# Kernel optimization log

Measured on AMD Instinct MI355X. Metric: run time of the kernel, lower is better.

Reference implementation:

```python
import jax, jax.numpy as jnp
import numpy as np

B, N = 4, 1024                 # images, proposals per image
C_IN, POOL, HID = 256, 7, 1024
NUM_CLASSES = 21               # 20 fg + background (include_bg=False => +1)
FEAT_DIM = C_IN * POOL * POOL  # 12544
IMAGE_H = IMAGE_W = 800.0
STDS = np.array([0.1, 0.1, 0.2, 0.2], np.float32)
SCORE_THRESH = 0.1
NMS_THRESH = 0.5


def setup_inputs():
    key = jax.random.key(0)
    ks = jax.random.split(key, 11)
    props_feature = jax.random.normal(ks[0], (B * N, FEAT_DIM), jnp.float32)
    # well-formed xyxy proposals inside the image
    xy = jax.random.uniform(ks[1], (B, N, 2), minval=0.0, maxval=IMAGE_W - 64.0)
    wh = jax.random.uniform(ks[2], (B, N, 2), minval=8.0, maxval=256.0)
    proposals = jnp.concatenate([xy, jnp.minimum(xy + wh, IMAGE_W)], axis=-1)
    s = 0.02
    return {
        'props_feature': props_feature,
        'proposals': proposals,
        'fc6_w': jax.random.normal(ks[3], (FEAT_DIM, HID), jnp.float32) * s,
        'fc6_b': jnp.zeros((HID,), jnp.float32),
        'fc7_w': jax.random.normal(ks[4], (HID, HID), jnp.float32) * s,
        'fc7_b': jnp.zeros((HID,), jnp.float32),
        'cls_w': jax.random.normal(ks[5], (HID, NUM_CLASSES), jnp.float32) * s,
        'cls_b': jnp.zeros((NUM_CLASSES,), jnp.float32),
        'box_w': jax.random.normal(ks[6], (HID, NUM_CLASSES * 4), jnp.float32) * s,
        'box_b': jnp.zeros((NUM_CLASSES * 4,), jnp.float32),
    }


def _decode(deltas, props):
    # NormalizedProposalDecoder: deltas [...,4] (normalized), props xyxy [...,4]
    d = deltas * jnp.asarray(STDS)  # means are 0
    w = props[..., 2] - props[..., 0]
    h = props[..., 3] - props[..., 1]
    cx = props[..., 0] + 0.5 * w
    cy = props[..., 1] + 0.5 * h
    pcx = d[..., 0] * w + cx
    pcy = d[..., 1] * h + cy
    pw = jnp.exp(d[..., 2]) * w
    ph = jnp.exp(d[..., 3]) * h
    return jnp.stack([pcx - 0.5 * pw, pcy - 0.5 * ph,
                      pcx + 0.5 * pw, pcy + 0.5 * ph], axis=-1)


def _pairwise_iou(a, b):
    lt = jnp.maximum(a[:, None, :2], b[None, :, :2])
    rb = jnp.minimum(a[:, None, 2:], b[None, :, 2:])
    wh = jnp.maximum(rb - lt, 0.0)
    inter = wh[..., 0] * wh[..., 1]
    area_a = (a[:, 2] - a[:, 0]) * (a[:, 3] - a[:, 1])
    area_b = (b[:, 2] - b[:, 0]) * (b[:, 3] - b[:, 1])
    return inter / jnp.maximum(area_a[:, None] + area_b[None, :] - inter, 1e-9)


def _nms_keep(boxes, scores, labels, valid):
    # torchvision batched_nms: per-class via coordinate offset trick
    sc = jnp.where(valid, scores, -1.0)
    order = jnp.argsort(-sc)
    off = labels[order].astype(boxes.dtype)[:, None] * (IMAGE_W + 1.0)
    b = boxes[order] + off
    iou = _pairwise_iou(b, b)  # [N, N]
    idx = jnp.arange(N)

    def body(i, keep):
        sup = (iou[i] > NMS_THRESH) & keep[i] & (idx > i)
        return keep & ~sup

    keep_sorted = jax.lax.fori_loop(0, N, body, valid[order])
    return jnp.zeros(N, bool).at[order].set(keep_sorted)


def reference(props_feature, proposals, fc6_w, fc6_b, fc7_w, fc7_b,
              cls_w, cls_b, box_w, box_b):
    # TwoMLPHead
    x = jax.nn.relu(props_feature @ fc6_w + fc6_b)
    x = jax.nn.relu(x @ fc7_w + fc7_b)
    # FastRCNNPredictor
    scores = jax.nn.softmax(x @ cls_w + cls_b, axis=-1).reshape(B, N, NUM_CLASSES)
    deltas = (x @ box_w + box_b).reshape(B, N, NUM_CLASSES, 4)
    boxes = _decode(deltas, proposals[:, :, None, :])  # [B,N,C,4]
    # drop background column, keep per-box max-score class (scores == max mask)
    sc_fg = scores[..., 1:]
    bx_fg = boxes[:, :, 1:, :]
    best = jnp.argmax(sc_fg, axis=-1)                                  # [B,N]
    sc = jnp.take_along_axis(sc_fg, best[..., None], axis=-1)[..., 0]
    bx = jnp.take_along_axis(bx_fg, best[..., None, None], axis=-2)[..., 0, :]
    labels = best + 1
    # BBoxClipToImageSize
    hi = jnp.asarray([IMAGE_W, IMAGE_H, IMAGE_W, IMAGE_H], bx.dtype)
    bx = jnp.clip(bx, jnp.zeros(4, bx.dtype), hi)
    # BBoxSizeFilter(min=0) + score threshold
    valid = ((bx[..., 2] - bx[..., 0] > 0.0) & (bx[..., 3] - bx[..., 1] > 0.0)
             & (sc > SCORE_THRESH))
    keep = jax.vmap(_nms_keep)(bx, sc, labels, valid)                  # [B,N]
    res = jnp.concatenate([bx, (labels - 1).astype(bx.dtype)[..., None],
                           sc[..., None]], axis=-1)                    # [B,N,6]
    res = jnp.where(keep[..., None], res, 0.0)  # padded in place of ragged lists
    rpn_props = jnp.pad(proposals, ((0, 0), (0, 0), (0, 2)))
    rcnn_props = jnp.pad(bx, ((0, 0), (0, 0), (0, 2)))
    return res, keep, rpn_props, rcnn_props
```

## Files before the change

### kernel.cpp

```cpp
#include <hip/hip_runtime.h>
#include <hip/hip_bf16.h>

#define BATCH 4
#define NPROP 1024
#define HID 1024
#define NUM_CLASSES 21
#define FEAT_DIM 12544
#define NPB (BATCH * NPROP)
#define IMG 800.0f
#define SCORE_THRESH 0.1f
#define NMS_THRESH 0.5f
#define NCOL 112

typedef unsigned short u16;
typedef unsigned int u32;
typedef unsigned long long u64;
typedef short s16x8 __attribute__((ext_vector_type(8)));
typedef float f32x4 __attribute__((ext_vector_type(4)));

__device__ __forceinline__ void split2(float x0, float x1, u32& hp, u32& lp) {
    __hip_bfloat162 h2 = __float22bfloat162_rn(make_float2(x0, x1));
    u32 h = *(u32*)&h2;
    float f0 = __uint_as_float(h << 16);
    float f1 = __uint_as_float(h & 0xffff0000u);
    __hip_bfloat162 l2 = __float22bfloat162_rn(make_float2(x0 - f0, x1 - f1));
    hp = h;
    lp = *(u32*)&l2;
}

__device__ __forceinline__ size_t tile_off(int blk, int NTt, int t, int row, int g) {
    int r = row & 127;
    int c = r >> 4;
    int lanei = ((r & 15) << 2) | (g ^ ((r >> 1) & 3));
    return ((((size_t)blk * NTt + t) * 8 + c) << 9) + lanei * 8;
}

__global__ __launch_bounds__(256) void transpose_split(
    const float* __restrict__ W, u16* __restrict__ WhT, u16* __restrict__ WlT,
    int K, int N)
{
    __shared__ float tile[32][33];
    const int tid = threadIdx.x;
    const int n0 = blockIdx.x * 32;
    const int k0 = blockIdx.y * 32;
    {
        int i = tid >> 3, j4 = (tid & 7) * 4;
        float4 v = *(const float4*)(W + (size_t)(k0 + i) * N + n0 + j4);
        tile[i][j4] = v.x; tile[i][j4 + 1] = v.y; tile[i][j4 + 2] = v.z; tile[i][j4 + 3] = v.w;
    }
    __syncthreads();
    {
        int i = tid >> 3, j4 = (tid & 7) * 4;
        u32 hp0, lp0, hp1, lp1;
        split2(tile[j4 + 0][i], tile[j4 + 1][i], hp0, lp0);
        split2(tile[j4 + 2][i], tile[j4 + 3][i], hp1, lp1);
        size_t o = (size_t)(n0 + i) * K + k0 + j4;
        *(uint2*)&WhT[o] = make_uint2(hp0, hp1);
        *(uint2*)&WlT[o] = make_uint2(lp0, lp1);
    }
}

__global__ __launch_bounds__(256) void transpose_split_tiled(
    const float* __restrict__ W, u16* __restrict__ Th, u16* __restrict__ Tl,
    int K, int N)
{
    __shared__ float tile[32][33];
    const int tid = threadIdx.x;
    const int n0 = blockIdx.x * 32;
    const int k0 = blockIdx.y * 32;
    {
        int i = tid >> 3, j4 = (tid & 7) * 4;
        float4 v = *(const float4*)(W + (size_t)(k0 + i) * N + n0 + j4);
        tile[i][j4] = v.x; tile[i][j4 + 1] = v.y; tile[i][j4 + 2] = v.z; tile[i][j4 + 3] = v.w;
    }
    __syncthreads();
    if (tid < 128) {
        const int nl = tid & 31, g = tid >> 5;
        const int n = n0 + nl;
        u32 hp[4], lp[4];
#pragma unroll
        for (int e2 = 0; e2 < 4; ++e2)
            split2(tile[g * 8 + e2 * 2][nl], tile[g * 8 + e2 * 2 + 1][nl], hp[e2], lp[e2]);
        size_t dsto = tile_off(n >> 7, K >> 5, k0 >> 5, n, g);
        *(uint4*)&Th[dsto] = make_uint4(hp[0], hp[1], hp[2], hp[3]);
        *(uint4*)&Tl[dsto] = make_uint4(lp[0], lp[1], lp[2], lp[3]);
    }
}

__global__ __launch_bounds__(256) void split_a_tiled(
    const float* __restrict__ A, u16* __restrict__ Ah, u16* __restrict__ Al,
    int K, long n8)
{
    const int NTt = K >> 5;
    for (long i = blockIdx.x * 256L + threadIdx.x; i < n8; i += (long)gridDim.x * 256L) {
        size_t o = (size_t)i * 8;
        int row = (int)(o / (size_t)K);
        int rem = (int)(o - (size_t)row * K);
        int t = rem >> 5;
        int g = (rem >> 3) & 3;
        float4 v0 = *(const float4*)(A + o);
        float4 v1 = *(const float4*)(A + o + 4);
        u32 hp[4], lp[4];
        split2(v0.x, v0.y, hp[0], lp[0]);
        split2(v0.z, v0.w, hp[1], lp[1]);
        split2(v1.x, v1.y, hp[2], lp[2]);
        split2(v1.z, v1.w, hp[3], lp[3]);
        size_t dsto = tile_off(row >> 7, NTt, t, row, g);
        *(uint4*)&Ah[dsto] = make_uint4(hp[0], hp[1], hp[2], hp[3]);
        *(uint4*)&Al[dsto] = make_uint4(lp[0], lp[1], lp[2], lp[3]);
    }
}

__global__ void build_wcat(const float* __restrict__ cls_w, const float* __restrict__ box_w,
                           float* __restrict__ Wcat)
{
    int i = blockIdx.x * 256 + threadIdx.x;
    if (i >= HID * NCOL) return;
    int k = i / NCOL, c = i % NCOL;
    float v = 0.0f;
    if (c < 21) v = cls_w[k * 21 + c];
    else if (c < 105) v = box_w[k * 84 + (c - 21)];
    Wcat[i] = v;
}

__global__ __launch_bounds__(256) void gemm_2ph_tiled(
    const u16* __restrict__ Ah, const u16* __restrict__ Al,
    const u16* __restrict__ Wh, const u16* __restrict__ Wl,
    const float* __restrict__ bias, float* __restrict__ Cout,
    int M, int Nn, int NTt, int tN)
{
    __shared__ u16 sm[2 * 16384];

    const int tid = threadIdx.x;
    const int lane = tid & 63;
    const int wv = tid >> 6;
    const int wr = wv >> 1, wc = wv & 1;

    const int flat = blockIdx.x + (blockIdx.y << 3) + (blockIdx.z << 8);
    const int xcd = flat & 7;
    const int j = flat >> 3;
    const int bxi = j & 7;
    const int yy = (j >> 3) & 3;
    const int bz = j >> 5;
    const int mb = xcd * 4 + yy;
    const int nb = bxi;
    const int bm = mb * 128, bn = nb * 128;
    const int t0 = bz * tN;

    const size_t abase = (size_t)mb * NTt * 4096;
    const size_t wbase = (size_t)nb * NTt * 4096;

    const int fr = lane & 15, fq = lane >> 4;
    int ia[4], ib[4];
#pragma unroll
    for (int m = 0; m < 4; ++m) {
        int ra = wr * 64 + m * 16 + fr;
        ia[m] = ra * 32 + ((fq ^ ((ra >> 1) & 3)) << 3);
        int rb = wc * 64 + m * 16 + fr;
        ib[m] = rb * 32 + ((fq ^ ((rb >> 1) & 3)) << 3);
    }

    f32x4 acc[4][4];
#pragma unroll
    for (int m = 0; m < 4; ++m)
#pragma unroll
        for (int n = 0; n < 4; ++n)
            acc[m][n] = (f32x4){0.f, 0.f, 0.f, 0.f};

    auto stage = [&](u16* dst, int t) {
#pragma unroll
        for (int i = 0; i < 2; ++i) {
            const int c = wv * 2 + i;
            const size_t so = (((size_t)t * 8 + c) << 9) + lane * 8;
            __builtin_amdgcn_global_load_lds(
                (const __attribute__((address_space(1))) u32*)(Ah + abase + so),
                (__attribute__((address_space(3))) u32*)(dst + c * 512), 16, 0, 0);
            __builtin_amdgcn_global_load_lds(
                (const __attribute__((address_space(1))) u32*)(Al + abase + so),
                (__attribute__((address_space(3))) u32*)(dst + 4096 + c * 512), 16, 0, 0);
            __builtin_amdgcn_global_load_lds(
                (const __attribute__((address_space(1))) u32*)(Wh + wbase + so),
                (__attribute__((address_space(3))) u32*)(dst + 8192 + c * 512), 16, 0, 0);
            __builtin_amdgcn_global_load_lds(
                (const __attribute__((address_space(1))) u32*)(Wl + wbase + so),
                (__attribute__((address_space(3))) u32*)(dst + 12288 + c * 512), 16, 0, 0);
        }
    };

    auto compute = [&](const u16* src) {
        s16x8 fah[4], fal[4], fbh[4], fbl[4];
#pragma unroll
        for (int m = 0; m < 4; ++m) {
            fah[m] = *(const s16x8*)&src[ia[m]];
            fal[m] = *(const s16x8*)&src[4096 + ia[m]];
            fbh[m] = *(const s16x8*)&src[8192 + ib[m]];
            fbl[m] = *(const s16x8*)&src[12288 + ib[m]];
        }
        __builtin_amdgcn_s_setprio(1);
#pragma unroll
        for (int m = 0; m < 4; ++m)
#pragma unroll
            for (int n = 0; n < 4; ++n) {
                acc[m][n] = __builtin_amdgcn_mfma_f32_16x16x32_bf16(fah[m], fbh[n], acc[m][n], 0, 0, 0);
                acc[m][n] = __builtin_amdgcn_mfma_f32_16x16x32_bf16(fah[m], fbl[n], acc[m][n], 0, 0, 0);
                acc[m][n] = __builtin_amdgcn_mfma_f32_16x16x32_bf16(fal[m], fbh[n], acc[m][n], 0, 0, 0);
            }
        __builtin_amdgcn_s_setprio(0);
    };

    u16* bufc = sm;
    u16* bufn = sm + 16384;

    stage(bufc, t0);
    for (int t = 0; t < tN; ++t) {
        if (t + 1 < tN) {
            stage(bufn, t0 + t + 1);
            asm volatile("s_waitcnt vmcnt(8)" ::: "memory");
        } else {
            asm volatile("s_waitcnt vmcnt(0)" ::: "memory");
        }
        asm volatile("s_barrier" ::: "memory");
        compute(bufc);
        asm volatile("s_barrier" ::: "memory");
        u16* tmp = bufc; bufc = bufn; bufn = tmp;
    }

    if (bias != nullptr) {
#pragma unroll
        for (int n = 0; n < 4; ++n) {
            int col = bn + wc * 64 + n * 16 + fr;
            float bb = bias[col];
#pragma unroll
            for (int m = 0; m < 4; ++m) {
                int row0 = bm + wr * 64 + m * 16 + fq * 4;
#pragma unroll
                for (int jj = 0; jj < 4; ++jj)
                    Cout[(size_t)(row0 + jj) * Nn + col] = fmaxf(acc[m][n][jj] + bb, 0.0f);
            }
        }
    } else {
        float* Cp = Cout + (size_t)bz * M * Nn;
#pragma unroll
        for (int n = 0; n < 4; ++n) {
            int col = bn + wc * 64 + n * 16 + fr;
#pragma unroll
            for (int m = 0; m < 4; ++m) {
                int row0 = bm + wr * 64 + m * 16 + fq * 4;
#pragma unroll
                for (int jj = 0; jj < 4; ++jj)
                    Cp[(size_t)(row0 + jj) * Nn + col] = acc[m][n][jj];
            }
        }
    }
}

__global__ __launch_bounds__(256) void gemm_2ph(
    const float* __restrict__ A, const u16* __restrict__ WhT, const u16* __restrict__ WlT,
    const float* __restrict__ bias, float* __restrict__ Cout,
    int M, int Nn, int K, int KC)
{
    __shared__ u16 sm[2 * 16384];

    const int tid = threadIdx.x;
    const int lane = tid & 63;
    const int wv = tid >> 6;
    const int wr = wv >> 1, wc = wv & 1;

    const int flat = blockIdx.x + (blockIdx.y << 3) + (blockIdx.z << 8);
    const int xcd = flat & 7;
    const int j = flat >> 3;
    const int bxi = j & 7;
    const int yy = (j >> 3) & 3;
    const int bz = j >> 5;
    const int bm = (xcd * 4 + yy) * 128;
    const int bn = bxi * 128;
    const int k0 = bz * KC;
    const int NT = KC / 32;

    const int ar = tid >> 1;
    const int ah = tid & 1;
    const float* aPtr = A + (size_t)(bm + ar) * K + ah * 16;
    const int asw = (ar >> 1) & 3;
    const int ac0 = ((2 * ah) ^ asw) << 3;
    const int ac1 = ((2 * ah + 1) ^ asw) << 3;

    int wrow[2], wlc[2];
#pragma unroll
    for (int i = 0; i < 2; ++i) {
        int c = wv * 2 + i;
        wrow[i] = c * 16 + (lane >> 2);
        wlc[i] = ((lane & 3) ^ ((wrow[i] >> 1) & 3)) * 8;
    }

    const int fr = lane & 15, fq = lane >> 4;
    int ia[4], ib[4];
#pragma unroll
    for (int m = 0; m < 4; ++m) {
        int ra = wr * 64 + m * 16 + fr;
        ia[m] = ra * 32 + ((fq ^ ((ra >> 1) & 3)) << 3);
        int rb = wc * 64 + m * 16 + fr;
        ib[m] = rb * 32 + ((fq ^ ((rb >> 1) & 3)) << 3);
    }

    f32x4 acc[4][4];
#pragma unroll
    for (int m = 0; m < 4; ++m)
#pragma unroll
        for (int n = 0; n < 4; ++n)
            acc[m][n] = (f32x4){0.f, 0.f, 0.f, 0.f};

    auto stage_w = [&](u16* dst, int kk) {
#pragma unroll
        for (int i = 0; i < 2; ++i) {
            const int c = wv * 2 + i;
            const u16* gh = WhT + (size_t)(bn + wrow[i]) * K + kk + wlc[i];
            const u16* gl = WlT + (size_t)(bn + wrow[i]) * K + kk + wlc[i];
            __builtin_amdgcn_global_load_lds(
                (const __attribute__((address_space(1))) u32*)gh,
                (__attribute__((address_space(3))) u32*)(dst + 8192 + c * 512), 16, 0, 0);
            __builtin_amdgcn_global_load_lds(
                (const __attribute__((address_space(1))) u32*)gl,
                (__attribute__((address_space(3))) u32*)(dst + 12288 + c * 512), 16, 0, 0);
        }
    };

    auto split_a = [&](u16* dst, float4 v0, float4 v1, float4 v2, float4 v3) {
        u32 hp[8], lp[8];
        split2(v0.x, v0.y, hp[0], lp[0]);
        split2(v0.z, v0.w, hp[1], lp[1]);
        split2(v1.x, v1.y, hp[2], lp[2]);
        split2(v1.z, v1.w, hp[3], lp[3]);
        split2(v2.x, v2.y, hp[4], lp[4]);
        split2(v2.z, v2.w, hp[5], lp[5]);
        split2(v3.x, v3.y, hp[6], lp[6]);
        split2(v3.z, v3.w, hp[7], lp[7]);
        *(uint4*)&dst[ar * 32 + ac0] = make_uint4(hp[0], hp[1], hp[2], hp[3]);
        *(uint4*)&dst[ar * 32 + ac1] = make_uint4(hp[4], hp[5], hp[6], hp[7]);
        *(uint4*)&dst[4096 + ar * 32 + ac0] = make_uint4(lp[0], lp[1], lp[2], lp[3]);
        *(uint4*)&dst[4096 + ar * 32 + ac1] = make_uint4(lp[4], lp[5], lp[6], lp[7]);
    };

    auto compute = [&](const u16* src) {
        s16x8 fah[4], fal[4], fbh[4], fbl[4];
#pragma unroll
        for (int m = 0; m < 4; ++m) {
            fah[m] = *(const s16x8*)&src[ia[m]];
            fal[m] = *(const s16x8*)&src[4096 + ia[m]];
            fbh[m] = *(const s16x8*)&src[8192 + ib[m]];
            fbl[m] = *(const s16x8*)&src[12288 + ib[m]];
        }
        __builtin_amdgcn_s_setprio(1);
#pragma unroll
        for (int m = 0; m < 4; ++m)
#pragma unroll
            for (int n = 0; n < 4; ++n) {
                acc[m][n] = __builtin_amdgcn_mfma_f32_16x16x32_bf16(fah[m], fbh[n], acc[m][n], 0, 0, 0);
                acc[m][n] = __builtin_amdgcn_mfma_f32_16x16x32_bf16(fah[m], fbl[n], acc[m][n], 0, 0, 0);
                acc[m][n] = __builtin_amdgcn_mfma_f32_16x16x32_bf16(fal[m], fbh[n], acc[m][n], 0, 0, 0);
            }
        __builtin_amdgcn_s_setprio(0);
    };

    u16* bufc = sm;
    u16* bufn = sm + 16384;

    stage_w(bufc, k0);
    {
        float4 a0 = *(const float4*)(aPtr + k0 + 0);
        float4 a1 = *(const float4*)(aPtr + k0 + 4);
        float4 a2 = *(const float4*)(aPtr + k0 + 8);
        float4 a3 = *(const float4*)(aPtr + k0 + 12);
        split_a(bufc, a0, a1, a2, a3);
    }
    asm volatile("s_waitcnt vmcnt(0) lgkmcnt(0)\n\ts_barrier" ::: "memory");

    for (int t = 0; t < NT; ++t) {
        float4 a0{}, a1{}, a2{}, a3{};
        const bool hn = (t + 1 < NT);
        if (hn) {
            const int kk = k0 + (t + 1) * 32;
            stage_w(bufn, kk);
            a0 = *(const float4*)(aPtr + kk + 0);
            a1 = *(const float4*)(aPtr + kk + 4);
            a2 = *(const float4*)(aPtr + kk + 8);
            a3 = *(const float4*)(aPtr + kk + 12);
        }
        compute(bufc);
        if (hn) split_a(bufn, a0, a1, a2, a3);
        asm volatile("s_waitcnt vmcnt(0) lgkmcnt(0)\n\ts_barrier" ::: "memory");
        u16* tmp = bufc; bufc = bufn; bufn = tmp;
    }

    if (bias != nullptr) {
#pragma unroll
        for (int n = 0; n < 4; ++n) {
            int col = bn + wc * 64 + n * 16 + fr;
            float bb = bias[col];
#pragma unroll
            for (int m = 0; m < 4; ++m) {
                int row0 = bm + wr * 64 + m * 16 + fq * 4;
#pragma unroll
                for (int jj = 0; jj < 4; ++jj)
                    Cout[(size_t)(row0 + jj) * Nn + col] = fmaxf(acc[m][n][jj] + bb, 0.0f);
            }
        }
    } else {
        float* Cp = Cout + (size_t)bz * M * Nn;
#pragma unroll
        for (int n = 0; n < 4; ++n) {
            int col = bn + wc * 64 + n * 16 + fr;
#pragma unroll
            for (int m = 0; m < 4; ++m) {
                int row0 = bm + wr * 64 + m * 16 + fq * 4;
#pragma unroll
                for (int jj = 0; jj < 4; ++jj)
                    Cp[(size_t)(row0 + jj) * Nn + col] = acc[m][n][jj];
            }
        }
    }
}

__global__ __launch_bounds__(256) void reduce_bias_relu(
    const float* __restrict__ Cpart, const float* __restrict__ bias,
    float* __restrict__ X, int MN, int Nn)
{
    const int total = MN / 4;
    for (int i4 = blockIdx.x * 256 + threadIdx.x; i4 < total; i4 += gridDim.x * 256) {
        const size_t o = (size_t)i4 * 4;
        float4 a = *(const float4*)(Cpart + o);
        float4 b = *(const float4*)(Cpart + (size_t)MN + o);
        float4 c = *(const float4*)(Cpart + 2 * (size_t)MN + o);
        float4 d = *(const float4*)(Cpart + 3 * (size_t)MN + o);
        float4 bb = *(const float4*)(bias + (o & (size_t)(Nn - 1)));
        float4 r;
        r.x = fmaxf(a.x + b.x + c.x + d.x + bb.x, 0.0f);
        r.y = fmaxf(a.y + b.y + c.y + d.y + bb.y, 0.0f);
        r.z = fmaxf(a.z + b.z + c.z + d.z + bb.z, 0.0f);
        r.w = fmaxf(a.w + b.w + c.w + d.w + bb.w, 0.0f);
        *(float4*)(X + o) = r;
    }
}

__global__ __launch_bounds__(256) void reduce_split_tiled(
    const float* __restrict__ Cpart, const float* __restrict__ bias,
    u16* __restrict__ Xh, u16* __restrict__ Xl, int MN, int Nn)
{
    const int total = MN / 8;
    for (int i = blockIdx.x * 256 + threadIdx.x; i < total; i += gridDim.x * 256) {
        const size_t o = (size_t)i * 8;
        float r8[8];
#pragma unroll
        for (int h = 0; h < 2; ++h) {
            float4 a = *(const float4*)(Cpart + o + h * 4);
            float4 b = *(const float4*)(Cpart + (size_t)MN + o + h * 4);
            float4 c = *(const float4*)(Cpart + 2 * (size_t)MN + o + h * 4);
            float4 d = *(const float4*)(Cpart + 3 * (size_t)MN + o + h * 4);
            float4 bb = *(const float4*)(bias + ((o + h * 4) & (size_t)(Nn - 1)));
            r8[h * 4 + 0] = fmaxf(a.x + b.x + c.x + d.x + bb.x, 0.0f);
            r8[h * 4 + 1] = fmaxf(a.y + b.y + c.y + d.y + bb.y, 0.0f);
            r8[h * 4 + 2] = fmaxf(a.z + b.z + c.z + d.z + bb.z, 0.0f);
            r8[h * 4 + 3] = fmaxf(a.w + b.w + c.w + d.w + bb.w, 0.0f);
        }
        u32 hp[4], lp[4];
#pragma unroll
        for (int t2 = 0; t2 < 4; ++t2)
            split2(r8[2 * t2], r8[2 * t2 + 1], hp[t2], lp[t2]);
        int row = (int)(o >> 10);
        int rem = (int)(o & 1023);
        int t = rem >> 5, g = (rem >> 3) & 3;
        size_t dsto = tile_off(row >> 7, 32, t, row, g);
        *(uint4*)&Xh[dsto] = make_uint4(hp[0], hp[1], hp[2], hp[3]);
        *(uint4*)&Xl[dsto] = make_uint4(lp[0], lp[1], lp[2], lp[3]);
    }
}

__global__ __launch_bounds__(256) void heads_gemm(
    const float* __restrict__ X2, const float* __restrict__ Wcat, float* __restrict__ logits)
{
    __shared__ float Xs[32][36];
    __shared__ float Ws[32 * NCOL];
    const int tid = threadIdx.x;
    const int m0 = blockIdx.x * 32;
    const int tr = tid >> 4;
    const int tc = tid & 15;
    float acc0[7] = {}, acc1[7] = {};
    for (int k0 = 0; k0 < HID; k0 += 32) {
        {
            int i = tid >> 3, j4 = (tid & 7) * 4;
            float4 v = *(const float4*)(X2 + (size_t)(m0 + i) * HID + k0 + j4);
            Xs[i][j4] = v.x; Xs[i][j4 + 1] = v.y; Xs[i][j4 + 2] = v.z; Xs[i][j4 + 3] = v.w;
        }
        const float4* src = (const float4*)(Wcat + (size_t)k0 * NCOL);
        float4* dst = (float4*)Ws;
        for (int i4 = tid; i4 < (32 * NCOL) / 4; i4 += 256) dst[i4] = src[i4];
        __syncthreads();
#pragma unroll 4
        for (int kk = 0; kk < 32; ++kk) {
            float a0 = Xs[tr][kk], a1 = Xs[tr + 16][kk];
#pragma unroll
            for (int j = 0; j < 7; ++j) {
                float b = Ws[kk * NCOL + tc * 7 + j];
                acc0[j] = fmaf(a0, b, acc0[j]);
                acc1[j] = fmaf(a1, b, acc1[j]);
            }
        }
        __syncthreads();
    }
#pragma unroll
    for (int j = 0; j < 7; ++j) {
        logits[(size_t)(m0 + tr) * NCOL + tc * 7 + j] = acc0[j];
        logits[(size_t)(m0 + tr + 16) * NCOL + tc * 7 + j] = acc1[j];
    }
}

__global__ __launch_bounds__(256) void postproc(
    const float* __restrict__ logits, const float* __restrict__ cls_b,
    const float* __restrict__ box_b, const float* __restrict__ proposals,
    float* __restrict__ bxo, float* __restrict__ sco,
    int* __restrict__ lbo, int* __restrict__ vdo)
{
    int p = blockIdx.x * 256 + threadIdx.x;
    if (p >= NPB) return;
    const float* lg = logits + (size_t)p * NCOL;
    float l[21];
    float m = -1e30f;
#pragma unroll
    for (int c = 0; c < 21; ++c) { l[c] = lg[c] + cls_b[c]; m = fmaxf(m, l[c]); }
    float e[21]; float s = 0.0f;
#pragma unroll
    for (int c = 0; c < 21; ++c) { e[c] = expf(l[c] - m); s += e[c]; }
    int best = 1;
#pragma unroll
    for (int c = 2; c < 21; ++c) if (e[c] > e[best]) best = c;
    const float score = e[best] / s;

    float d0 = (lg[21 + best * 4 + 0] + box_b[best * 4 + 0]) * 0.1f;
    float d1 = (lg[21 + best * 4 + 1] + box_b[best * 4 + 1]) * 0.1f;
    float d2 = (lg[21 + best * 4 + 2] + box_b[best * 4 + 2]) * 0.2f;
    float d3 = (lg[21 + best * 4 + 3] + box_b[best * 4 + 3]) * 0.2f;
    const float* pr = proposals + p * 4;
    float w_ = pr[2] - pr[0], h_ = pr[3] - pr[1];
    float cx = pr[0] + 0.5f * w_, cy = pr[1] + 0.5f * h_;
    float pcx = d0 * w_ + cx, pcy = d1 * h_ + cy;
    float pw = expf(d2) * w_, ph = expf(d3) * h_;
    float b0 = pcx - 0.5f * pw, b1 = pcy - 0.5f * ph;
    float b2 = pcx + 0.5f * pw, b3 = pcy + 0.5f * ph;
    b0 = fminf(fmaxf(b0, 0.0f), IMG);
    b1 = fminf(fmaxf(b1, 0.0f), IMG);
    b2 = fminf(fmaxf(b2, 0.0f), IMG);
    b3 = fminf(fmaxf(b3, 0.0f), IMG);
    int vd = (b2 - b0 > 0.0f) && (b3 - b1 > 0.0f) && (score > SCORE_THRESH);
    bxo[p * 4 + 0] = b0; bxo[p * 4 + 1] = b1;
    bxo[p * 4 + 2] = b2; bxo[p * 4 + 3] = b3;
    sco[p] = score;
    lbo[p] = best;
    vdo[p] = vd;
}

__global__ __launch_bounds__(1024) void nms_kernel(
    const float* __restrict__ bx, const float* __restrict__ sc,
    const int* __restrict__ label, const int* __restrict__ valid,
    int* __restrict__ keepg)
{
    const int img = blockIdx.x;
    const int base = img * NPROP;
    const int tid = threadIdx.x;

    __shared__ u64 maskm[NPROP][16];
    __shared__ float4 sbx[NPROP];
    __shared__ float sarea[NPROP];
    __shared__ unsigned char skeep[NPROP];
    __shared__ u64 kword[16];
    __shared__ int nv;

    u64* skey = &maskm[0][0];

    if (tid == 0) nv = 0;

    {
        float s = valid[base + tid] ? sc[base + tid] : -1.0f;
        unsigned u = __float_as_uint(s);
        u = (u & 0x80000000u) ? ~u : (u | 0x80000000u);
        u = ~u;
        skey[tid] = ((u64)u << 32) | (unsigned)tid;
    }
    for (int k = 2; k <= NPROP; k <<= 1) {
        for (int j = k >> 1; j > 0; j >>= 1) {
            __syncthreads();
            int ixj = tid ^ j;
            if (ixj > tid) {
                u64 a = skey[tid], b = skey[ixj];
                bool up = ((tid & k) == 0);
                if (up ? (a > b) : (a < b)) { skey[tid] = b; skey[ixj] = a; }
            }
        }
    }
    __syncthreads();

    const int myp = (int)(skey[tid] & 0xffffffffu);
    {
        float off = (float)label[base + myp] * (IMG + 1.0f);
        float x0 = bx[(base + myp) * 4 + 0] + off;
        float y0 = bx[(base + myp) * 4 + 1] + off;
        float x1 = bx[(base + myp) * 4 + 2] + off;
        float y1 = bx[(base + myp) * 4 + 3] + off;
        sbx[tid] = make_float4(x0, y0, x1, y1);
        sarea[tid] = (x1 - x0) * (y1 - y0);
        int v = valid[base + myp];
        skeep[tid] = (unsigned char)v;
        if (v) atomicMax(&nv, tid + 1);
    }
    __syncthreads();
    const int nvalid = nv;

    for (int idx = tid; idx < nvalid * 16; idx += 1024) {
        const int i = idx >> 4, w = idx & 15;
        const float4 bi = sbx[i];
        const float ai = sarea[i];
        u64 bits = 0;
        const int jlo = w * 64;
        const int jhi = min(jlo + 64, nvalid);
        for (int j = max(jlo, i + 1); j < jhi; ++j) {
            float4 bj = sbx[j];
            float lt0 = fmaxf(bi.x, bj.x);
            float lt1 = fmaxf(bi.y, bj.y);
            float rb0 = fminf(bi.z, bj.z);
            float rb1 = fminf(bi.w, bj.w);
            float w_ = fmaxf(rb0 - lt0, 0.0f);
            float h_ = fmaxf(rb1 - lt1, 0.0f);
            float inter = w_ * h_;
            float denom = fmaxf(ai + sarea[j] - inter, 1e-9f);
            if (inter / denom > NMS_THRESH) bits |= 1ull << (j - jlo);
        }
        maskm[i][w] = bits;
    }
    if (tid < 16) {
        u64 kw = 0;
        for (int b = 0; b < 64; ++b)
            kw |= (u64)(skeep[tid * 64 + b] ? 1 : 0) << b;
        kword[tid] = kw;
    }
    __syncthreads();

    if (tid < 64) {
        u64 kw = (tid < 16) ? kword[tid] : 0ull;
        for (int i = 0; i < nvalid; ++i) {
            u64 srcw = __shfl(kw, i >> 6, 64);
            if ((srcw >> (i & 63)) & 1ull) {
                if (tid < 16) kw &= ~maskm[i][tid];
            }
        }
        if (tid < 16) kword[tid] = kw;
    }
    __syncthreads();

    keepg[base + myp] = (int)((kword[tid >> 6] >> (tid & 63)) & 1ull);
}

__global__ __launch_bounds__(256) void finalize_kernel(
    const float* __restrict__ bx, const float* __restrict__ sc,
    const int* __restrict__ label, const int* __restrict__ keepg,
    const float* __restrict__ proposals, float* __restrict__ out)
{
    const int p = blockIdx.x * blockDim.x + threadIdx.x;
    if (p >= NPB) return;
    float* res = out;
    float* keepo = out + NPB * 6;
    float* rpn = keepo + NPB;
    float* rcnn = rpn + NPB * 6;
    const bool k = keepg[p] != 0;
    float b0 = bx[p * 4 + 0], b1 = bx[p * 4 + 1];
    float b2 = bx[p * 4 + 2], b3 = bx[p * 4 + 3];
    res[p * 6 + 0] = k ? b0 : 0.0f;
    res[p * 6 + 1] = k ? b1 : 0.0f;
    res[p * 6 + 2] = k ? b2 : 0.0f;
    res[p * 6 + 3] = k ? b3 : 0.0f;
    res[p * 6 + 4] = k ? (float)(label[p] - 1) : 0.0f;
    res[p * 6 + 5] = k ? sc[p] : 0.0f;
    keepo[p] = k ? 1.0f : 0.0f;
    rpn[p * 6 + 0] = proposals[p * 4 + 0];
    rpn[p * 6 + 1] = proposals[p * 4 + 1];
    rpn[p * 6 + 2] = proposals[p * 4 + 2];
    rpn[p * 6 + 3] = proposals[p * 4 + 3];
    rpn[p * 6 + 4] = 0.0f;
    rpn[p * 6 + 5] = 0.0f;
    rcnn[p * 6 + 0] = b0;
    rcnn[p * 6 + 1] = b1;
    rcnn[p * 6 + 2] = b2;
    rcnn[p * 6 + 3] = b3;
    rcnn[p * 6 + 4] = 0.0f;
    rcnn[p * 6 + 5] = 0.0f;
}

extern "C" void kernel_launch(void* const* d_in, const int* in_sizes, int n_in,
                              void* d_out, int out_size, void* d_ws, size_t ws_size,
                              hipStream_t stream)
{
    const float* props_feature = (const float*)d_in[0];
    const float* proposals     = (const float*)d_in[1];
    const float* fc6_w         = (const float*)d_in[2];
    const float* fc6_b         = (const float*)d_in[3];
    const float* fc7_w         = (const float*)d_in[4];
    const float* fc7_b         = (const float*)d_in[5];
    const float* cls_w         = (const float*)d_in[6];
    const float* cls_b         = (const float*)d_in[7];
    const float* box_w         = (const float*)d_in[8];
    const float* box_b         = (const float*)d_in[9];
    float* out = (float*)d_out;

    char* ws = (char*)d_ws;
    float* X1     = (float*)(ws);
    float* X2     = (float*)(ws + 16777216);
    float* Wcat   = (float*)(ws + 33554432);
    float* logits = (float*)(ws + 34013184);
    float* bx     = (float*)(ws + 35848192);
    float* sc     = (float*)(ws + 35913728);
    int*   label  = (int*)  (ws + 35930112);
    int*   valid  = (int*)  (ws + 35946496);
    int*   keepg  = (int*)  (ws + 35962880);
    u16*   W6h    = (u16*)  (ws + 35979264);
    u16*   W6l    = (u16*)  (ws + 61669376);
    u16*   W7h    = (u16*)  (ws + 87359488);
    u16*   W7l    = (u16*)  (ws + 89456640);
    float* Cpart  = (float*)(ws + 91553792);
    u16*   A6h    = (u16*)  (ws + 158662656);
    u16*   A6l    = (u16*)  (ws + 261423104);
    u16*   X1h    = (u16*)  (ws + 364183552);
    u16*   X1l    = (u16*)  (ws + 372572160);
    const size_t NEED_SK   = 158662656ull;
    const size_t NEED_FULL = 380960768ull;

    build_wcat<<<(HID * NCOL + 255) / 256, 256, 0, stream>>>(cls_w, box_w, Wcat);

    if (ws_size >= NEED_FULL) {
        transpose_split_tiled<<<dim3(HID / 32, FEAT_DIM / 32), 256, 0, stream>>>(
            fc6_w, W6h, W6l, FEAT_DIM, HID);
        transpose_split_tiled<<<dim3(HID / 32, HID / 32), 256, 0, stream>>>(
            fc7_w, W7h, W7l, HID, HID);
        split_a_tiled<<<2048, 256, 0, stream>>>(
            props_feature, A6h, A6l, FEAT_DIM, (long)NPB * FEAT_DIM / 8);
        gemm_2ph_tiled<<<dim3(8, 32, 4), 256, 0, stream>>>(
            A6h, A6l, W6h, W6l, nullptr, Cpart, NPB, HID, FEAT_DIM / 32, FEAT_DIM / 128);
        reduce_split_tiled<<<1024, 256, 0, stream>>>(
            Cpart, fc6_b, X1h, X1l, NPB * HID, HID);
        gemm_2ph_tiled<<<dim3(8, 32, 1), 256, 0, stream>>>(
            X1h, X1l, W7h, W7l, fc7_b, X2, NPB, HID, HID / 32, HID / 32);
    } else if (ws_size >= NEED_SK) {
        transpose_split<<<dim3(HID / 32, FEAT_DIM / 32), 256, 0, stream>>>(
            fc6_w, W6h, W6l, FEAT_DIM, HID);
        transpose_split<<<dim3(HID / 32, HID / 32), 256, 0, stream>>>(
            fc7_w, W7h, W7l, HID, HID);
        gemm_2ph<<<dim3(8, 32, 4), 256, 0, stream>>>(
            props_feature, W6h, W6l, nullptr, Cpart, NPB, HID, FEAT_DIM, FEAT_DIM / 4);
        reduce_bias_relu<<<1024, 256, 0, stream>>>(Cpart, fc6_b, X1, NPB * HID, HID);
        gemm_2ph<<<dim3(8, 32, 1), 256, 0, stream>>>(
            X1, W7h, W7l, fc7_b, X2, NPB, HID, HID, HID);
    } else {
        transpose_split<<<dim3(HID / 32, FEAT_DIM / 32), 256, 0, stream>>>(
            fc6_w, W6h, W6l, FEAT_DIM, HID);
        transpose_split<<<dim3(HID / 32, HID / 32), 256, 0, stream>>>(
            fc7_w, W7h, W7l, HID, HID);
        gemm_2ph<<<dim3(8, 32, 1), 256, 0, stream>>>(
            props_feature, W6h, W6l, fc6_b, X1, NPB, HID, FEAT_DIM, FEAT_DIM);
        gemm_2ph<<<dim3(8, 32, 1), 256, 0, stream>>>(
            X1, W7h, W7l, fc7_b, X2, NPB, HID, HID, HID);
    }

    heads_gemm<<<NPB / 32, 256, 0, stream>>>(X2, Wcat, logits);
    postproc<<<NPB / 256, 256, 0, stream>>>(logits, cls_b, box_b, proposals,
                                            bx, sc, label, valid);

    nms_kernel<<<BATCH, 1024, 0, stream>>>(bx, sc, label, valid, keepg);
    finalize_kernel<<<(NPB + 255) / 256, 256, 0, stream>>>(
        bx, sc, label, keepg, proposals, out);
}
```

Before: 720.7 us.

## Fuse prep kernels, heads with postproc, and NMS with finalize

Merges the wcat build, both weight transpose-splits and the activation split into one prep kernel that picks its role from the block index. Fuses the heads GEMM with postprocessing through shared-memory logits, and folds the output writing into the NMS kernel. This removes several launches and the global round-trips of logits and keep flags. The trade-off is that postproc now runs on only 32 threads per block, and finalize runs on just 4 blocks of 1024 threads.

```diff
diff --git a/kernel.cpp b/kernel.cpp
--- a/kernel.cpp
+++ b/kernel.cpp
@@ -35,6 +35,89 @@
     return ((((size_t)blk * NTt + t) * 8 + c) << 9) + lanei * 8;
 }
 
+#define NB_WCAT 448
+#define NB_T7   1024
+#define NB_T6   12544
+#define NB_SPA  2048
+#define NB_PREP (NB_WCAT + NB_T7 + NB_T6 + NB_SPA)
+
+__device__ __forceinline__ void transpose_tiled_body(
+    const float* __restrict__ W, u16* __restrict__ Th, u16* __restrict__ Tl,
+    int K, int N, int bx, int by, int tid, float (*tile)[33])
+{
+    const int n0 = bx * 32;
+    const int k0 = by * 32;
+    {
+        int i = tid >> 3, j4 = (tid & 7) * 4;
+        float4 v = *(const float4*)(W + (size_t)(k0 + i) * N + n0 + j4);
+        tile[i][j4] = v.x; tile[i][j4 + 1] = v.y; tile[i][j4 + 2] = v.z; tile[i][j4 + 3] = v.w;
+    }
+    __syncthreads();
+    if (tid < 128) {
+        const int nl = tid & 31, g = tid >> 5;
+        const int n = n0 + nl;
+        u32 hp[4], lp[4];
+#pragma unroll
+        for (int e2 = 0; e2 < 4; ++e2)
+            split2(tile[g * 8 + e2 * 2][nl], tile[g * 8 + e2 * 2 + 1][nl], hp[e2], lp[e2]);
+        size_t dsto = tile_off(n >> 7, K >> 5, k0 >> 5, n, g);
+        *(uint4*)&Th[dsto] = make_uint4(hp[0], hp[1], hp[2], hp[3]);
+        *(uint4*)&Tl[dsto] = make_uint4(lp[0], lp[1], lp[2], lp[3]);
+    }
+}
+
+__global__ __launch_bounds__(256) void prep_kernel(
+    const float* __restrict__ fc6_w, const float* __restrict__ fc7_w,
+    const float* __restrict__ cls_w, const float* __restrict__ box_w,
+    const float* __restrict__ A,
+    u16* __restrict__ W6h, u16* __restrict__ W6l,
+    u16* __restrict__ W7h, u16* __restrict__ W7l,
+    float* __restrict__ Wcat, u16* __restrict__ A6h, u16* __restrict__ A6l)
+{
+    __shared__ float tile[32][33];
+    const int b = blockIdx.x;
+    const int tid = threadIdx.x;
+
+    if (b < NB_WCAT) {
+        int i = b * 256 + tid;
+        if (i < HID * NCOL) {
+            int k = i / NCOL, c = i % NCOL;
+            float v = 0.0f;
+            if (c < 21) v = cls_w[k * 21 + c];
+            else if (c < 105) v = box_w[k * 84 + (c - 21)];
+            Wcat[i] = v;
+        }
+    } else if (b < NB_WCAT + NB_T7) {
+        int idx = b - NB_WCAT;
+        transpose_tiled_body(fc7_w, W7h, W7l, HID, HID, idx & 31, idx >> 5, tid, tile);
+    } else if (b < NB_WCAT + NB_T7 + NB_T6) {
+        int idx = b - NB_WCAT - NB_T7;
+        transpose_tiled_body(fc6_w, W6h, W6l, FEAT_DIM, HID, idx & 31, idx >> 5, tid, tile);
+    } else {
+        const int sb = b - NB_WCAT - NB_T7 - NB_T6;
+        const long n8 = (long)NPB * FEAT_DIM / 8;
+        const int K = FEAT_DIM;
+        const int NTt = K >> 5;
+        for (long i = sb * 256L + tid; i < n8; i += (long)NB_SPA * 256L) {
+            size_t o = (size_t)i * 8;
+            int row = (int)(o / (size_t)K);
+            int rem = (int)(o - (size_t)row * K);
+            int t = rem >> 5;
+            int g = (rem >> 3) & 3;
+            float4 v0 = *(const float4*)(A + o);
+            float4 v1 = *(const float4*)(A + o + 4);
+            u32 hp[4], lp[4];
+            split2(v0.x, v0.y, hp[0], lp[0]);
+            split2(v0.z, v0.w, hp[1], lp[1]);
+            split2(v1.x, v1.y, hp[2], lp[2]);
+            split2(v1.z, v1.w, hp[3], lp[3]);
+            size_t dsto = tile_off(row >> 7, NTt, t, row, g);
+            *(uint4*)&A6h[dsto] = make_uint4(hp[0], hp[1], hp[2], hp[3]);
+            *(uint4*)&A6l[dsto] = make_uint4(lp[0], lp[1], lp[2], lp[3]);
+        }
+    }
+}
+
 __global__ __launch_bounds__(256) void transpose_split(
     const float* __restrict__ W, u16* __restrict__ WhT, u16* __restrict__ WlT,
     int K, int N)
@@ -57,57 +140,6 @@
         size_t o = (size_t)(n0 + i) * K + k0 + j4;
         *(uint2*)&WhT[o] = make_uint2(hp0, hp1);
         *(uint2*)&WlT[o] = make_uint2(lp0, lp1);
-    }
-}
-
-__global__ __launch_bounds__(256) void transpose_split_tiled(
-    const float* __restrict__ W, u16* __restrict__ Th, u16* __restrict__ Tl,
-    int K, int N)
-{
-    __shared__ float tile[32][33];
-    const int tid = threadIdx.x;
-    const int n0 = blockIdx.x * 32;
-    const int k0 = blockIdx.y * 32;
-    {
-        int i = tid >> 3, j4 = (tid & 7) * 4;
-        float4 v = *(const float4*)(W + (size_t)(k0 + i) * N + n0 + j4);
-        tile[i][j4] = v.x; tile[i][j4 + 1] = v.y; tile[i][j4 + 2] = v.z; tile[i][j4 + 3] = v.w;
-    }
-    __syncthreads();
-    if (tid < 128) {
-        const int nl = tid & 31, g = tid >> 5;
-        const int n = n0 + nl;
-        u32 hp[4], lp[4];
-#pragma unroll
-        for (int e2 = 0; e2 < 4; ++e2)
-            split2(tile[g * 8 + e2 * 2][nl], tile[g * 8 + e2 * 2 + 1][nl], hp[e2], lp[e2]);
-        size_t dsto = tile_off(n >> 7, K >> 5, k0 >> 5, n, g);
-        *(uint4*)&Th[dsto] = make_uint4(hp[0], hp[1], hp[2], hp[3]);
-        *(uint4*)&Tl[dsto] = make_uint4(lp[0], lp[1], lp[2], lp[3]);
-    }
-}
-
-__global__ __launch_bounds__(256) void split_a_tiled(
-    const float* __restrict__ A, u16* __restrict__ Ah, u16* __restrict__ Al,
-    int K, long n8)
-{
-    const int NTt = K >> 5;
-    for (long i = blockIdx.x * 256L + threadIdx.x; i < n8; i += (long)gridDim.x * 256L) {
-        size_t o = (size_t)i * 8;
-        int row = (int)(o / (size_t)K);
-        int rem = (int)(o - (size_t)row * K);
-        int t = rem >> 5;
-        int g = (rem >> 3) & 3;
-        float4 v0 = *(const float4*)(A + o);
-        float4 v1 = *(const float4*)(A + o + 4);
-        u32 hp[4], lp[4];
-        split2(v0.x, v0.y, hp[0], lp[0]);
-        split2(v0.z, v0.w, hp[1], lp[1]);
-        split2(v1.x, v1.y, hp[2], lp[2]);
-        split2(v1.z, v1.w, hp[3], lp[3]);
-        size_t dsto = tile_off(row >> 7, NTt, t, row, g);
-        *(uint4*)&Ah[dsto] = make_uint4(hp[0], hp[1], hp[2], hp[3]);
-        *(uint4*)&Al[dsto] = make_uint4(lp[0], lp[1], lp[2], lp[3]);
     }
 }
 
@@ -474,11 +506,16 @@
     }
 }
 
-__global__ __launch_bounds__(256) void heads_gemm(
-    const float* __restrict__ X2, const float* __restrict__ Wcat, float* __restrict__ logits)
+__global__ __launch_bounds__(256) void heads_postproc(
+    const float* __restrict__ X2, const float* __restrict__ Wcat,
+    const float* __restrict__ cls_b, const float* __restrict__ box_b,
+    const float* __restrict__ proposals,
+    float* __restrict__ bxo, float* __restrict__ sco,
+    int* __restrict__ lbo, int* __restrict__ vdo)
 {
     __shared__ float Xs[32][36];
     __shared__ float Ws[32 * NCOL];
+    __shared__ float lgs[32][NCOL];
     const int tid = threadIdx.x;
     const int m0 = blockIdx.x * 32;
     const int tr = tid >> 4;
@@ -508,59 +545,54 @@
     }
 #pragma unroll
     for (int j = 0; j < 7; ++j) {
-        logits[(size_t)(m0 + tr) * NCOL + tc * 7 + j] = acc0[j];
-        logits[(size_t)(m0 + tr + 16) * NCOL + tc * 7 + j] = acc1[j];
-    }
-}
-
-__global__ __launch_bounds__(256) void postproc(
-    const float* __restrict__ logits, const float* __restrict__ cls_b,
-    const float* __restrict__ box_b, const float* __restrict__ proposals,
-    float* __restrict__ bxo, float* __restrict__ sco,
-    int* __restrict__ lbo, int* __restrict__ vdo)
-{
-    int p = blockIdx.x * 256 + threadIdx.x;
-    if (p >= NPB) return;
-    const float* lg = logits + (size_t)p * NCOL;
-    float l[21];
-    float m = -1e30f;
-#pragma unroll
-    for (int c = 0; c < 21; ++c) { l[c] = lg[c] + cls_b[c]; m = fmaxf(m, l[c]); }
-    float e[21]; float s = 0.0f;
-#pragma unroll
-    for (int c = 0; c < 21; ++c) { e[c] = expf(l[c] - m); s += e[c]; }
-    int best = 1;
-#pragma unroll
-    for (int c = 2; c < 21; ++c) if (e[c] > e[best]) best = c;
-    const float score = e[best] / s;
-
-    float d0 = (lg[21 + best * 4 + 0] + box_b[best * 4 + 0]) * 0.1f;
-    float d1 = (lg[21 + best * 4 + 1] + box_b[best * 4 + 1]) * 0.1f;
-    float d2 = (lg[21 + best * 4 + 2] + box_b[best * 4 + 2]) * 0.2f;
-    float d3 = (lg[21 + best * 4 + 3] + box_b[best * 4 + 3]) * 0.2f;
-    const float* pr = proposals + p * 4;
-    float w_ = pr[2] - pr[0], h_ = pr[3] - pr[1];
-    float cx = pr[0] + 0.5f * w_, cy = pr[1] + 0.5f * h_;
-    float pcx = d0 * w_ + cx, pcy = d1 * h_ + cy;
-    float pw = expf(d2) * w_, ph = expf(d3) * h_;
-    float b0 = pcx - 0.5f * pw, b1 = pcy - 0.5f * ph;
-    float b2 = pcx + 0.5f * pw, b3 = pcy + 0.5f * ph;
-    b0 = fminf(fmaxf(b0, 0.0f), IMG);
-    b1 = fminf(fmaxf(b1, 0.0f), IMG);
-    b2 = fminf(fmaxf(b2, 0.0f), IMG);
-    b3 = fminf(fmaxf(b3, 0.0f), IMG);
-    int vd = (b2 - b0 > 0.0f) && (b3 - b1 > 0.0f) && (score > SCORE_THRESH);
-    bxo[p * 4 + 0] = b0; bxo[p * 4 + 1] = b1;
-    bxo[p * 4 + 2] = b2; bxo[p * 4 + 3] = b3;
-    sco[p] = score;
-    lbo[p] = best;
-    vdo[p] = vd;
-}
-
-__global__ __launch_bounds__(1024) void nms_kernel(
+        lgs[tr][tc * 7 + j] = acc0[j];
+        lgs[tr + 16][tc * 7 + j] = acc1[j];
+    }
+    __syncthreads();
+
+    if (tid < 32) {
+        const int p = m0 + tid;
+        const float* lg = lgs[tid];
+        float l[21];
+        float m = -1e30f;
+#pragma unroll
+        for (int c = 0; c < 21; ++c) { l[c] = lg[c] + cls_b[c]; m = fmaxf(m, l[c]); }
+        float e[21]; float s = 0.0f;
+#pragma unroll
+        for (int c = 0; c < 21; ++c) { e[c] = expf(l[c] - m); s += e[c]; }
+        int best = 1;
+#pragma unroll
+        for (int c = 2; c < 21; ++c) if (e[c] > e[best]) best = c;
+        const float score = e[best] / s;
+
+        float d0 = (lg[21 + best * 4 + 0] + box_b[best * 4 + 0]) * 0.1f;
+        float d1 = (lg[21 + best * 4 + 1] + box_b[best * 4 + 1]) * 0.1f;
+        float d2 = (lg[21 + best * 4 + 2] + box_b[best * 4 + 2]) * 0.2f;
+        float d3 = (lg[21 + best * 4 + 3] + box_b[best * 4 + 3]) * 0.2f;
+        const float* pr = proposals + p * 4;
+        float w_ = pr[2] - pr[0], h_ = pr[3] - pr[1];
+        float cx = pr[0] + 0.5f * w_, cy = pr[1] + 0.5f * h_;
+        float pcx = d0 * w_ + cx, pcy = d1 * h_ + cy;
+        float pw = expf(d2) * w_, ph = expf(d3) * h_;
+        float b0 = pcx - 0.5f * pw, b1 = pcy - 0.5f * ph;
+        float b2 = pcx + 0.5f * pw, b3 = pcy + 0.5f * ph;
+        b0 = fminf(fmaxf(b0, 0.0f), IMG);
+        b1 = fminf(fmaxf(b1, 0.0f), IMG);
+        b2 = fminf(fmaxf(b2, 0.0f), IMG);
+        b3 = fminf(fmaxf(b3, 0.0f), IMG);
+        int vd = (b2 - b0 > 0.0f) && (b3 - b1 > 0.0f) && (score > SCORE_THRESH);
+        bxo[p * 4 + 0] = b0; bxo[p * 4 + 1] = b1;
+        bxo[p * 4 + 2] = b2; bxo[p * 4 + 3] = b3;
+        sco[p] = score;
+        lbo[p] = best;
+        vdo[p] = vd;
+    }
+}
+
+__global__ __launch_bounds__(1024) void nms_finalize(
     const float* __restrict__ bx, const float* __restrict__ sc,
     const int* __restrict__ label, const int* __restrict__ valid,
-    int* __restrict__ keepg)
+    const float* __restrict__ proposals, float* __restrict__ out)
 {
     const int img = blockIdx.x;
     const int base = img * NPROP;
@@ -654,42 +686,35 @@
     }
     __syncthreads();
 
-    keepg[base + myp] = (int)((kword[tid >> 6] >> (tid & 63)) & 1ull);
-}
-
-__global__ __launch_bounds__(256) void finalize_kernel(
-    const float* __restrict__ bx, const float* __restrict__ sc,
-    const int* __restrict__ label, const int* __restrict__ keepg,
-    const float* __restrict__ proposals, float* __restrict__ out)
-{
-    const int p = blockIdx.x * blockDim.x + threadIdx.x;
-    if (p >= NPB) return;
-    float* res = out;
-    float* keepo = out + NPB * 6;
-    float* rpn = keepo + NPB;
-    float* rcnn = rpn + NPB * 6;
-    const bool k = keepg[p] != 0;
-    float b0 = bx[p * 4 + 0], b1 = bx[p * 4 + 1];
-    float b2 = bx[p * 4 + 2], b3 = bx[p * 4 + 3];
-    res[p * 6 + 0] = k ? b0 : 0.0f;
-    res[p * 6 + 1] = k ? b1 : 0.0f;
-    res[p * 6 + 2] = k ? b2 : 0.0f;
-    res[p * 6 + 3] = k ? b3 : 0.0f;
-    res[p * 6 + 4] = k ? (float)(label[p] - 1) : 0.0f;
-    res[p * 6 + 5] = k ? sc[p] : 0.0f;
-    keepo[p] = k ? 1.0f : 0.0f;
-    rpn[p * 6 + 0] = proposals[p * 4 + 0];
-    rpn[p * 6 + 1] = proposals[p * 4 + 1];
-    rpn[p * 6 + 2] = proposals[p * 4 + 2];
-    rpn[p * 6 + 3] = proposals[p * 4 + 3];
-    rpn[p * 6 + 4] = 0.0f;
-    rpn[p * 6 + 5] = 0.0f;
-    rcnn[p * 6 + 0] = b0;
-    rcnn[p * 6 + 1] = b1;
-    rcnn[p * 6 + 2] = b2;
-    rcnn[p * 6 + 3] = b3;
-    rcnn[p * 6 + 4] = 0.0f;
-    rcnn[p * 6 + 5] = 0.0f;
+    {
+        const int p = base + myp;
+        const bool k = ((kword[tid >> 6] >> (tid & 63)) & 1ull) != 0;
+        float* res   = out;
+        float* keepo = out + NPB * 6;
+        float* rpn   = keepo + NPB;
+        float* rcnn  = rpn + NPB * 6;
+        float b0 = bx[p * 4 + 0], b1 = bx[p * 4 + 1];
+        float b2 = bx[p * 4 + 2], b3 = bx[p * 4 + 3];
+        res[p * 6 + 0] = k ? b0 : 0.0f;
+        res[p * 6 + 1] = k ? b1 : 0.0f;
+        res[p * 6 + 2] = k ? b2 : 0.0f;
+        res[p * 6 + 3] = k ? b3 : 0.0f;
+        res[p * 6 + 4] = k ? (float)(label[p] - 1) : 0.0f;
+        res[p * 6 + 5] = k ? sc[p] : 0.0f;
+        keepo[p] = k ? 1.0f : 0.0f;
+        rpn[p * 6 + 0] = proposals[p * 4 + 0];
+        rpn[p * 6 + 1] = proposals[p * 4 + 1];
+        rpn[p * 6 + 2] = proposals[p * 4 + 2];
+        rpn[p * 6 + 3] = proposals[p * 4 + 3];
+        rpn[p * 6 + 4] = 0.0f;
+        rpn[p * 6 + 5] = 0.0f;
+        rcnn[p * 6 + 0] = b0;
+        rcnn[p * 6 + 1] = b1;
+        rcnn[p * 6 + 2] = b2;
+        rcnn[p * 6 + 3] = b3;
+        rcnn[p * 6 + 4] = 0.0f;
+        rcnn[p * 6 + 5] = 0.0f;
+    }
 }
 
 extern "C" void kernel_launch(void* const* d_in, const int* in_sizes, int n_in,
@@ -712,12 +737,10 @@
     float* X1     = (float*)(ws);
     float* X2     = (float*)(ws + 16777216);
     float* Wcat   = (float*)(ws + 33554432);
-    float* logits = (float*)(ws + 34013184);
     float* bx     = (float*)(ws + 35848192);
     float* sc     = (float*)(ws + 35913728);
     int*   label  = (int*)  (ws + 35930112);
     int*   valid  = (int*)  (ws + 35946496);
-    int*   keepg  = (int*)  (ws + 35962880);
     u16*   W6h    = (u16*)  (ws + 35979264);
     u16*   W6l    = (u16*)  (ws + 61669376);
     u16*   W7h    = (u16*)  (ws + 87359488);
@@ -730,15 +753,10 @@
     const size_t NEED_SK   = 158662656ull;
     const size_t NEED_FULL = 380960768ull;
 
-    build_wcat<<<(HID * NCOL + 255) / 256, 256, 0, stream>>>(cls_w, box_w, Wcat);
-
     if (ws_size >= NEED_FULL) {
-        transpose_split_tiled<<<dim3(HID / 32, FEAT_DIM / 32), 256, 0, stream>>>(
-            fc6_w, W6h, W6l, FEAT_DIM, HID);
-        transpose_split_tiled<<<dim3(HID / 32, HID / 32), 256, 0, stream>>>(
-            fc7_w, W7h, W7l, HID, HID);
-        split_a_tiled<<<2048, 256, 0, stream>>>(
-            props_feature, A6h, A6l, FEAT_DIM, (long)NPB * FEAT_DIM / 8);
+        prep_kernel<<<NB_PREP, 256, 0, stream>>>(
+            fc6_w, fc7_w, cls_w, box_w, props_feature,
+            W6h, W6l, W7h, W7l, Wcat, A6h, A6l);
         gemm_2ph_tiled<<<dim3(8, 32, 4), 256, 0, stream>>>(
             A6h, A6l, W6h, W6l, nullptr, Cpart, NPB, HID, FEAT_DIM / 32, FEAT_DIM / 128);
         reduce_split_tiled<<<1024, 256, 0, stream>>>(
@@ -746,6 +764,7 @@
         gemm_2ph_tiled<<<dim3(8, 32, 1), 256, 0, stream>>>(
             X1h, X1l, W7h, W7l, fc7_b, X2, NPB, HID, HID / 32, HID / 32);
     } else if (ws_size >= NEED_SK) {
+        build_wcat<<<(HID * NCOL + 255) / 256, 256, 0, stream>>>(cls_w, box_w, Wcat);
         transpose_split<<<dim3(HID / 32, FEAT_DIM / 32), 256, 0, stream>>>(
             fc6_w, W6h, W6l, FEAT_DIM, HID);
         transpose_split<<<dim3(HID / 32, HID / 32), 256, 0, stream>>>(
@@ -756,6 +775,7 @@
         gemm_2ph<<<dim3(8, 32, 1), 256, 0, stream>>>(
             X1, W7h, W7l, fc7_b, X2, NPB, HID, HID, HID);
     } else {
+        build_wcat<<<(HID * NCOL + 255) / 256, 256, 0, stream>>>(cls_w, box_w, Wcat);
         transpose_split<<<dim3(HID / 32, FEAT_DIM / 32), 256, 0, stream>>>(
             fc6_w, W6h, W6l, FEAT_DIM, HID);
         transpose_split<<<dim3(HID / 32, HID / 32), 256, 0, stream>>>(
@@ -766,11 +786,8 @@
             X1, W7h, W7l, fc7_b, X2, NPB, HID, HID, HID);
     }
 
-    heads_gemm<<<NPB / 32, 256, 0, stream>>>(X2, Wcat, logits);
-    postproc<<<NPB / 256, 256, 0, stream>>>(logits, cls_b, box_b, proposals,
-                                            bx, sc, label, valid);
-
-    nms_kernel<<<BATCH, 1024, 0, stream>>>(bx, sc, label, valid, keepg);
-    finalize_kernel<<<(NPB + 255) / 256, 256, 0, stream>>>(
-        bx, sc, label, keepg, proposals, out);
-}
+    heads_postproc<<<NPB / 32, 256, 0, stream>>>(
+        X2, Wcat, cls_b, box_b, proposals, bx, sc, label, valid);
+
+    nms_finalize<<<BATCH, 1024, 0, stream>>>(bx, sc, label, valid, proposals, out);
+}
```

Result: no change. 711.2 us (-1.3%).
